# Kernel optimization log

Measured on AMD Instinct MI355X. Metric: run time of the kernel, lower is better.

## Reference

```python
import jax, jax.numpy as jnp
import numpy as np

SEQ, BATCH, NFEAT, HID = 512, 128, 64, 256


def setup_inputs() -> dict:
    key = jax.random.key(0)
    ks = jax.random.split(key, 11)
    s = 0.05
    return {
        "X": jax.random.normal(ks[0], (SEQ, BATCH, NFEAT), jnp.float32),
        "w_ih0": jax.random.normal(ks[1], (4 * HID, NFEAT), jnp.float32) * s,
        "w_hh0": jax.random.normal(ks[2], (4 * HID, HID), jnp.float32) * s,
        "b_ih0": jax.random.normal(ks[3], (4 * HID,), jnp.float32) * s,
        "b_hh0": jax.random.normal(ks[4], (4 * HID,), jnp.float32) * s,
        "w_ih1": jax.random.normal(ks[5], (4 * HID, HID), jnp.float32) * s,
        "w_hh1": jax.random.normal(ks[6], (4 * HID, HID), jnp.float32) * s,
        "b_ih1": jax.random.normal(ks[7], (4 * HID,), jnp.float32) * s,
        "b_hh1": jax.random.normal(ks[8], (4 * HID,), jnp.float32) * s,
        "fc_w": jax.random.normal(ks[9], (1, HID), jnp.float32) * s,
        "fc_b": jax.random.normal(ks[10], (1,), jnp.float32) * s,
    }


def _lstm_layer(x, w_ih, w_hh, b_ih, b_hh):
    # x: [S, B, F]; PyTorch gate order: i, f, g, o along the 4H axis.
    S, B, _ = x.shape
    H = w_hh.shape[1]
    # Precompute input projection for all timesteps (batched GEMM).
    xp = jnp.einsum("sbf,gf->sbg", x, w_ih) + b_ih + b_hh  # [S, B, 4H]
    w_hh_t = w_hh.T  # [H, 4H]

    def step(carry, xt):
        h, c = carry
        gates = xt + h @ w_hh_t  # [B, 4H]
        i, f, g, o = jnp.split(gates, 4, axis=-1)
        i = jax.nn.sigmoid(i)
        f = jax.nn.sigmoid(f)
        g = jnp.tanh(g)
        o = jax.nn.sigmoid(o)
        c = f * c + i * g
        h = o * jnp.tanh(c)
        return (h, c), h

    h0 = jnp.zeros((B, H), x.dtype)
    c0 = jnp.zeros((B, H), x.dtype)
    _, out = jax.lax.scan(step, (h0, c0), xp)
    return out  # [S, B, H]


def reference(X, w_ih0, w_hh0, b_ih0, b_hh0, w_ih1, w_hh1, b_ih1, b_hh1, fc_w, fc_b):
    out0 = _lstm_layer(X, w_ih0, w_hh0, b_ih0, b_hh0)
    out1 = _lstm_layer(out0, w_ih1, w_hh1, b_ih1, b_hh1)
    last = out1[-1]  # [B, H]
    return last @ fc_w.T + fc_b  # [B, 1]
```

## Files before the change

kernel.cpp:

```cpp
#include <hip/hip_runtime.h>

#define SEQ   512
#define BATCH 128
#define NFEAT 64
#define HID   256
#define HB    (BATCH * HID)
#define NGRP  8
#define GBLK  32


typedef __attribute__((ext_vector_type(8))) short  short8;
typedef __attribute__((ext_vector_type(4))) float  f32x4;
typedef __attribute__((ext_vector_type(4))) unsigned short us4;

__device__ __forceinline__ unsigned short f2bf(float f) {
    union { float f; unsigned u; } c; c.f = f;
    unsigned r = c.u + 0x7FFF + ((c.u >> 16) & 1);
    return (unsigned short)(r >> 16);
}
__device__ __forceinline__ float bf2f(unsigned short h) {
    union { float f; unsigned u; } c; c.u = ((unsigned)h) << 16;
    return c.f;
}

__device__ __forceinline__ float2 aload2(const float* p) {
    unsigned long long raw = __hip_atomic_load(
        (const unsigned long long*)p, __ATOMIC_RELAXED, __HIP_MEMORY_SCOPE_AGENT);
    union { unsigned long long u; float2 f; } c; c.u = raw;
    return c.f;
}
__device__ __forceinline__ void astore1(float* p, float v) {
    union { float f; unsigned u; } c; c.f = v;
    __hip_atomic_store((unsigned*)p, c.u, __ATOMIC_RELAXED, __HIP_MEMORY_SCOPE_AGENT);
}

__global__ __launch_bounds__(256, 1) void lstm_persist(
    const float* __restrict__ X,
    const float* __restrict__ w_ih0,
    const float* __restrict__ w_hh0,
    const float* __restrict__ b_ih0,
    const float* __restrict__ b_hh0,
    const float* __restrict__ w_ih1,
    const float* __restrict__ w_hh1,
    const float* __restrict__ b_ih1,
    const float* __restrict__ b_hh1,
    float* __restrict__ h0buf,
    float* __restrict__ h1buf,
    unsigned* __restrict__ flags)
{
    const int bid = blockIdx.x;
    const int tid = threadIdx.x;
    const int g     = bid >> 5;
    const int r     = bid & 31;
    const int layer = r >> 4;
    const int ct    = r & 15;
    const int b0    = g * 16;
    const int j0    = ct * 16;

    const int wave = tid >> 6;
    const int l    = tid & 63;
    const int kq   = l >> 4;
    const int ar   = l & 15;

    __shared__ __align__(16) unsigned short hsh[16 * 512];
    __shared__ __align__(16) unsigned short hsl[16 * 512];
    __shared__ float red[4][4][16][17];
    __shared__ float bbuf[4][16];

    {
        const short8 z8 = {0, 0, 0, 0, 0, 0, 0, 0};
        for (int i = tid; i < 16 * 512 / 8; i += 256) {
            ((short8*)hsh)[i] = z8;
            ((short8*)hsl)[i] = z8;
        }
    }
    if (tid < 64) {
        const int gg = tid >> 4, cc = tid & 15;
        const float* bi_ = layer ? b_ih1 : b_ih0;
        const float* bh_ = layer ? b_hh1 : b_hh0;
        bbuf[gg][cc] = bi_[gg * 256 + j0 + cc] + bh_[gg * 256 + j0 + cc];
    }

    short8 Ahi[4][4], Alo[4][4];
    {
        const short8 z8 = {0, 0, 0, 0, 0, 0, 0, 0};
        #pragma unroll
        for (int gg = 0; gg < 4; ++gg) {
            const int row = gg * 256 + j0 + ar;
            #pragma unroll
            for (int kt = 0; kt < 4; ++kt) {
                const int k = (wave * 4 + kt) * 32 + kq * 8;
                const float* src = nullptr;
                if (layer) {
                    src = (k < 256) ? (w_ih1 + (size_t)row * 256 + k)
                                    : (w_hh1 + (size_t)row * 256 + (k - 256));
                } else {
                    if (k < 64)       src = w_ih0 + (size_t)row * 64 + k;
                    else if (k < 320) src = w_hh0 + (size_t)row * 256 + (k - 64);
                }
                short8 hi8 = z8, lo8 = z8;
                if (src) {
                    const float4 a = ((const float4*)src)[0];
                    const float4 b = ((const float4*)src)[1];
                    const float wv[8] = {a.x, a.y, a.z, a.w, b.x, b.y, b.z, b.w};
                    #pragma unroll
                    for (int i = 0; i < 8; ++i) {
                        const unsigned short h = f2bf(wv[i]);
                        hi8[i] = (short)h;
                        lo8[i] = (short)f2bf(wv[i] - bf2f(h));
                    }
                }
                Ahi[gg][kt] = hi8;
                Alo[gg][kt] = lo8;
            }
        }
    }

    const int eb = tid >> 4, ecc = tid & 15;
    float creg = 0.f;

    float*    hown  = layer ? h1buf : h0buf;
    unsigned* gflag = flags + (size_t)g * GBLK * 32;

    const int pb = tid >> 4, pf = tid & 15;
    float4 xpf = make_float4(0.f, 0.f, 0.f, 0.f);
    if (!layer)
        xpf = ((const float4*)(X + (size_t)(b0 + pb) * NFEAT))[pf];

    __syncthreads();

    for (int s = 0; s <= SEQ; ++s) {
        const int  t      = layer ? (s - 1) : s;
        const bool active = layer ? (s >= 1) : (s < SEQ);

        if (active) {
            const int par = t & 1;
            const int row = tid >> 4, f0 = tid & 15;
            const int swz = (row & 7) << 3;
            {
                const int hoff = layer ? 256 : 64;
                const float* hp =
                    hown + (size_t)(par ^ 1) * HB + (size_t)(b0 + row) * HID + f0 * 16;
                float v[16];
                #pragma unroll
                for (int i = 0; i < 8; ++i) {
                    const float2 t2 = aload2(hp + 2 * i);
                    v[2 * i] = t2.x; v[2 * i + 1] = t2.y;
                }
                short8 h0v, h1v, l0v, l1v;
                #pragma unroll
                for (int i = 0; i < 8; ++i) {
                    unsigned short hh = f2bf(v[i]);
                    h0v[i] = (short)hh;
                    l0v[i] = (short)f2bf(v[i] - bf2f(hh));
                    hh = f2bf(v[i + 8]);
                    h1v[i] = (short)hh;
                    l1v[i] = (short)f2bf(v[i + 8] - bf2f(hh));
                }
                const int us = row * 512 + hoff + f0 * 16;
                *(short8*)&hsh[us ^ swz]       = h0v;
                *(short8*)&hsh[(us + 8) ^ swz] = h1v;
                *(short8*)&hsl[us ^ swz]       = l0v;
                *(short8*)&hsl[(us + 8) ^ swz] = l1v;
            }
            if (layer) {
                const float* xp =
                    h0buf + (size_t)par * HB + (size_t)(b0 + row) * HID + f0 * 16;
                float v[16];
                #pragma unroll
                for (int i = 0; i < 8; ++i) {
                    const float2 t2 = aload2(xp + 2 * i);
                    v[2 * i] = t2.x; v[2 * i + 1] = t2.y;
                }
                short8 h0v, h1v, l0v, l1v;
                #pragma unroll
                for (int i = 0; i < 8; ++i) {
                    unsigned short hh = f2bf(v[i]);
                    h0v[i] = (short)hh;
                    l0v[i] = (short)f2bf(v[i] - bf2f(hh));
                    hh = f2bf(v[i + 8]);
                    h1v[i] = (short)hh;
                    l1v[i] = (short)f2bf(v[i + 8] - bf2f(hh));
                }
                const int us = row * 512 + f0 * 16;
                *(short8*)&hsh[us ^ swz]       = h0v;
                *(short8*)&hsh[(us + 8) ^ swz] = h1v;
                *(short8*)&hsl[us ^ swz]       = l0v;
                *(short8*)&hsl[(us + 8) ^ swz] = l1v;
            } else {
                const float xv[4] = {xpf.x, xpf.y, xpf.z, xpf.w};
                us4 xh, xl;
                #pragma unroll
                for (int i = 0; i < 4; ++i) {
                    const unsigned short hh = f2bf(xv[i]);
                    xh[i] = hh;
                    xl[i] = f2bf(xv[i] - bf2f(hh));
                }
                const int us = pb * 512 + pf * 4;
                const int sw = (pb & 7) << 3;
                *(us4*)&hsh[us ^ sw] = xh;
                *(us4*)&hsl[us ^ sw] = xl;
            }
        }
        __syncthreads();

        if (!layer && t + 1 < SEQ)
            xpf = ((const float4*)(X + (size_t)(t + 1) * BATCH * NFEAT
                                     + (size_t)(b0 + pb) * NFEAT))[pf];

        if (active) {
            f32x4 acc[4];
            #pragma unroll
            for (int gg = 0; gg < 4; ++gg)
                acc[gg] = (f32x4){0.f, 0.f, 0.f, 0.f};

            #pragma unroll
            for (int kt = 0; kt < 4; ++kt) {
                const int KT = wave * 4 + kt;
                const int us = ar * 512 + KT * 32 + kq * 8;
                const int uswz = us ^ ((ar & 7) << 3);
                const short8 bh = *(const short8*)&hsh[uswz];
                const short8 bl = *(const short8*)&hsl[uswz];
                #pragma unroll
                for (int gg = 0; gg < 4; ++gg)
                    acc[gg] = __builtin_amdgcn_mfma_f32_16x16x32_bf16(
                        Ahi[gg][kt], bh, acc[gg], 0, 0, 0);
                #pragma unroll
                for (int gg = 0; gg < 4; ++gg)
                    acc[gg] = __builtin_amdgcn_mfma_f32_16x16x32_bf16(
                        Alo[gg][kt], bh, acc[gg], 0, 0, 0);
                #pragma unroll
                for (int gg = 0; gg < 4; ++gg)
                    acc[gg] = __builtin_amdgcn_mfma_f32_16x16x32_bf16(
                        Ahi[gg][kt], bl, acc[gg], 0, 0, 0);
            }
            const int crow = kq * 4;
            #pragma unroll
            for (int gg = 0; gg < 4; ++gg) {
                #pragma unroll
                for (int i = 0; i < 4; ++i)
                    red[wave][gg][crow + i][ar] = acc[gg][i];
            }
        }
        __syncthreads();

        if (active) {
            float p[4];
            #pragma unroll
            for (int gg = 0; gg < 4; ++gg)
                p[gg] = bbuf[gg][ecc] + red[0][gg][ecc][eb] + red[1][gg][ecc][eb]
                                      + red[2][gg][ecc][eb] + red[3][gg][ecc][eb];
            const float ig = 1.0f / (1.0f + __expf(-p[0]));
            const float fg = 1.0f / (1.0f + __expf(-p[1]));
            const float gg_ = tanhf(p[2]);
            const float og = 1.0f / (1.0f + __expf(-p[3]));
            creg = fg * creg + ig * gg_;
            const float hv = og * tanhf(creg);
            astore1(&hown[(size_t)(t & 1) * HB + (size_t)(b0 + eb) * HID + j0 + ecc], hv);
        }

        if (s < SEQ) {
            const unsigned rr = (unsigned)(s + 1);
            __syncthreads();
            if (tid == 0)
                __hip_atomic_store(&gflag[r * 32], rr, __ATOMIC_RELAXED,
                                   __HIP_MEMORY_SCOPE_AGENT);
            if (tid < GBLK) {
                int guard = 0;
                while (__hip_atomic_load(&gflag[tid * 32], __ATOMIC_RELAXED,
                                         __HIP_MEMORY_SCOPE_AGENT) < rr &&
                       ++guard < (1 << 26))
                    __builtin_amdgcn_s_sleep(1);
            }
            __syncthreads();
        }
    }
}

__global__ __launch_bounds__(64) void fc_kernel(
    const float* __restrict__ h1last,
    const float* __restrict__ fc_w,
    const float* __restrict__ fc_b,
    float* __restrict__ out)
{
    const int b    = blockIdx.x;
    const int lane = threadIdx.x;
    float sum = 0.0f;
    #pragma unroll
    for (int k = lane; k < HID; k += 64)
        sum += h1last[b * HID + k] * fc_w[k];
    #pragma unroll
    for (int off = 32; off > 0; off >>= 1)
        sum += __shfl_down(sum, off);
    if (lane == 0) out[b] = sum + fc_b[0];
}

extern "C" void kernel_launch(void* const* d_in, const int* in_sizes, int n_in,
                              void* d_out, int out_size, void* d_ws, size_t ws_size,
                              hipStream_t stream)
{
    const float* X     = (const float*)d_in[0];
    const float* w_ih0 = (const float*)d_in[1];
    const float* w_hh0 = (const float*)d_in[2];
    const float* b_ih0 = (const float*)d_in[3];
    const float* b_hh0 = (const float*)d_in[4];
    const float* w_ih1 = (const float*)d_in[5];
    const float* w_hh1 = (const float*)d_in[6];
    const float* b_ih1 = (const float*)d_in[7];
    const float* b_hh1 = (const float*)d_in[8];
    const float* fc_w  = (const float*)d_in[9];
    const float* fc_b  = (const float*)d_in[10];

    float*    ws    = (float*)d_ws;
    float*    h0    = ws;
    float*    h1    = ws + 2 * HB;
    unsigned* flags = (unsigned*)(ws + 4 * HB);

    const size_t zbytes = (size_t)4 * HB * sizeof(float) + NGRP * GBLK * 32 * 4;
    (void)hipMemsetAsync(d_ws, 0, zbytes, stream);

    lstm_persist<<<NGRP * GBLK, 256, 0, stream>>>(X,
        w_ih0, w_hh0, b_ih0, b_hh0,
        w_ih1, w_hh1, b_ih1, b_hh1,
        h0, h1, flags);

    fc_kernel<<<BATCH, 64, 0, stream>>>(h1 + HB, fc_w, fc_b, (float*)d_out);
}
```

Measured before the change: 2.208 ms.

## Replace group-wide flag barrier with tagged hidden-state words and dataflow waits

Removes the per-step all-block flag barrier across the 32 blocks of a batch group. Each hidden value is now stored as a 64-bit word holding the step tag and the bf16 hi/lo split. Consumers spin until every loaded word carries the expected tag, so each block waits only on the data it reads. Layer 0 waits on a small layer-1 progress counter before overwriting its double buffer, and the hi/lo conversion moves to the producer. The LDS reduction layout is also changed to allow vector writes. Risks include heavier polling traffic on the h buffers, twice the buffer size, and correctness depending on relaxed 64-bit atomic visibility and bounded spin guards.

```diff
diff --git a/kernel.cpp b/kernel.cpp
--- a/kernel.cpp
+++ b/kernel.cpp
@@ -6,9 +6,9 @@
 #define HID   256
 #define HB    (BATCH * HID)
 #define NGRP  8
-#define GBLK  32
-
-
+
+
+typedef unsigned long long u64;
 typedef __attribute__((ext_vector_type(8))) short  short8;
 typedef __attribute__((ext_vector_type(4))) float  f32x4;
 typedef __attribute__((ext_vector_type(4))) unsigned short us4;
@@ -23,15 +23,17 @@
     return c.f;
 }
 
-__device__ __forceinline__ float2 aload2(const float* p) {
-    unsigned long long raw = __hip_atomic_load(
-        (const unsigned long long*)p, __ATOMIC_RELAXED, __HIP_MEMORY_SCOPE_AGENT);
-    union { unsigned long long u; float2 f; } c; c.u = raw;
-    return c.f;
-}
-__device__ __forceinline__ void astore1(float* p, float v) {
-    union { float f; unsigned u; } c; c.f = v;
-    __hip_atomic_store((unsigned*)p, c.u, __ATOMIC_RELAXED, __HIP_MEMORY_SCOPE_AGENT);
+__device__ __forceinline__ u64 ald64(const u64* p) {
+    return __hip_atomic_load(p, __ATOMIC_RELAXED, __HIP_MEMORY_SCOPE_AGENT);
+}
+__device__ __forceinline__ void ast64(u64* p, u64 v) {
+    __hip_atomic_store(p, v, __ATOMIC_RELAXED, __HIP_MEMORY_SCOPE_AGENT);
+}
+__device__ __forceinline__ unsigned ald32(const unsigned* p) {
+    return __hip_atomic_load(p, __ATOMIC_RELAXED, __HIP_MEMORY_SCOPE_AGENT);
+}
+__device__ __forceinline__ void ast32(unsigned* p, unsigned v) {
+    __hip_atomic_store(p, v, __ATOMIC_RELAXED, __HIP_MEMORY_SCOPE_AGENT);
 }
 
 __global__ __launch_bounds__(256, 1) void lstm_persist(
@@ -44,9 +46,9 @@
     const float* __restrict__ w_hh1,
     const float* __restrict__ b_ih1,
     const float* __restrict__ b_hh1,
-    float* __restrict__ h0buf,
-    float* __restrict__ h1buf,
-    unsigned* __restrict__ flags)
+    u64* __restrict__ h0w,
+    u64* __restrict__ h1w,
+    unsigned* __restrict__ l1prog)
 {
     const int bid = blockIdx.x;
     const int tid = threadIdx.x;
@@ -64,7 +66,7 @@
 
     __shared__ __align__(16) unsigned short hsh[16 * 512];
     __shared__ __align__(16) unsigned short hsl[16 * 512];
-    __shared__ float red[4][4][16][17];
+    __shared__ float red[4][4][16][20];
     __shared__ float bbuf[4][16];
 
     {
@@ -119,8 +121,9 @@
     const int eb = tid >> 4, ecc = tid & 15;
     float creg = 0.f;
 
-    float*    hown  = layer ? h1buf : h0buf;
-    unsigned* gflag = flags + (size_t)g * GBLK * 32;
+    u64*      hown = layer ? h1w : h0w;
+    unsigned* prog = l1prog + (size_t)g * 16 * 32;
+    const int hoff = layer ? 256 : 64;
 
     const int pb = tid >> 4, pf = tid & 15;
     float4 xpf = make_float4(0.f, 0.f, 0.f, 0.f);
@@ -129,86 +132,86 @@
 
     __syncthreads();
 
-    for (int s = 0; s <= SEQ; ++s) {
-        const int  t      = layer ? (s - 1) : s;
-        const bool active = layer ? (s >= 1) : (s < SEQ);
-
-        if (active) {
-            const int par = t & 1;
-            const int row = tid >> 4, f0 = tid & 15;
-            const int swz = (row & 7) << 3;
-            {
-                const int hoff = layer ? 256 : 64;
-                const float* hp =
-                    hown + (size_t)(par ^ 1) * HB + (size_t)(b0 + row) * HID + f0 * 16;
-                float v[16];
-                #pragma unroll
-                for (int i = 0; i < 8; ++i) {
-                    const float2 t2 = aload2(hp + 2 * i);
-                    v[2 * i] = t2.x; v[2 * i + 1] = t2.y;
-                }
-                short8 h0v, h1v, l0v, l1v;
-                #pragma unroll
-                for (int i = 0; i < 8; ++i) {
-                    unsigned short hh = f2bf(v[i]);
-                    h0v[i] = (short)hh;
-                    l0v[i] = (short)f2bf(v[i] - bf2f(hh));
-                    hh = f2bf(v[i + 8]);
-                    h1v[i] = (short)hh;
-                    l1v[i] = (short)f2bf(v[i + 8] - bf2f(hh));
-                }
-                const int us = row * 512 + hoff + f0 * 16;
-                *(short8*)&hsh[us ^ swz]       = h0v;
-                *(short8*)&hsh[(us + 8) ^ swz] = h1v;
-                *(short8*)&hsl[us ^ swz]       = l0v;
-                *(short8*)&hsl[(us + 8) ^ swz] = l1v;
-            }
-            if (layer) {
-                const float* xp =
-                    h0buf + (size_t)par * HB + (size_t)(b0 + row) * HID + f0 * 16;
-                float v[16];
-                #pragma unroll
-                for (int i = 0; i < 8; ++i) {
-                    const float2 t2 = aload2(xp + 2 * i);
-                    v[2 * i] = t2.x; v[2 * i + 1] = t2.y;
-                }
-                short8 h0v, h1v, l0v, l1v;
-                #pragma unroll
-                for (int i = 0; i < 8; ++i) {
-                    unsigned short hh = f2bf(v[i]);
-                    h0v[i] = (short)hh;
-                    l0v[i] = (short)f2bf(v[i] - bf2f(hh));
-                    hh = f2bf(v[i + 8]);
-                    h1v[i] = (short)hh;
-                    l1v[i] = (short)f2bf(v[i + 8] - bf2f(hh));
-                }
-                const int us = row * 512 + f0 * 16;
-                *(short8*)&hsh[us ^ swz]       = h0v;
-                *(short8*)&hsh[(us + 8) ^ swz] = h1v;
-                *(short8*)&hsl[us ^ swz]       = l0v;
-                *(short8*)&hsl[(us + 8) ^ swz] = l1v;
-            } else {
-                const float xv[4] = {xpf.x, xpf.y, xpf.z, xpf.w};
-                us4 xh, xl;
-                #pragma unroll
-                for (int i = 0; i < 4; ++i) {
-                    const unsigned short hh = f2bf(xv[i]);
-                    xh[i] = hh;
-                    xl[i] = f2bf(xv[i] - bf2f(hh));
-                }
-                const int us = pb * 512 + pf * 4;
-                const int sw = (pb & 7) << 3;
-                *(us4*)&hsh[us ^ sw] = xh;
-                *(us4*)&hsl[us ^ sw] = xl;
-            }
+    for (int t = 0; t < SEQ; ++t) {
+        const int par = t & 1, pp = par ^ 1;
+        const int b = tid >> 4, f0 = tid & 15;
+        const int swz = (b & 7) << 3;
+
+        if (t > 0) {
+            const u64* src = hown + ((size_t)pp * BATCH + b0 + b) * HID + f0 * 16;
+            u64 v[16];
+            const unsigned wtag = (unsigned)t;
+            int guard = 0; bool ok;
+            do {
+                ok = true;
+                #pragma unroll
+                for (int i = 0; i < 16; ++i) v[i] = ald64(src + i);
+                #pragma unroll
+                for (int i = 0; i < 16; ++i) ok &= ((unsigned)(v[i] >> 32) == wtag);
+            } while (!ok && ++guard < (1 << 16));
+            short8 h0v, h1v, l0v, l1v;
+            #pragma unroll
+            for (int i = 0; i < 8; ++i) {
+                h0v[i] = (short)((v[i] >> 16) & 0xffff);
+                l0v[i] = (short)(v[i] & 0xffff);
+                h1v[i] = (short)((v[i + 8] >> 16) & 0xffff);
+                l1v[i] = (short)(v[i + 8] & 0xffff);
+            }
+            const int us = b * 512 + hoff + f0 * 16;
+            *(short8*)&hsh[us ^ swz]       = h0v;
+            *(short8*)&hsh[(us + 8) ^ swz] = h1v;
+            *(short8*)&hsl[us ^ swz]       = l0v;
+            *(short8*)&hsl[(us + 8) ^ swz] = l1v;
+        }
+        if (layer) {
+            const u64* src = h0w + ((size_t)par * BATCH + b0 + b) * HID + f0 * 16;
+            u64 v[16];
+            const unsigned wtag = (unsigned)(t + 1);
+            int guard = 0; bool ok;
+            do {
+                ok = true;
+                #pragma unroll
+                for (int i = 0; i < 16; ++i) v[i] = ald64(src + i);
+                #pragma unroll
+                for (int i = 0; i < 16; ++i) ok &= ((unsigned)(v[i] >> 32) == wtag);
+            } while (!ok && ++guard < (1 << 16));
+            short8 h0v, h1v, l0v, l1v;
+            #pragma unroll
+            for (int i = 0; i < 8; ++i) {
+                h0v[i] = (short)((v[i] >> 16) & 0xffff);
+                l0v[i] = (short)(v[i] & 0xffff);
+                h1v[i] = (short)((v[i + 8] >> 16) & 0xffff);
+                l1v[i] = (short)(v[i + 8] & 0xffff);
+            }
+            const int us = b * 512 + f0 * 16;
+            *(short8*)&hsh[us ^ swz]       = h0v;
+            *(short8*)&hsh[(us + 8) ^ swz] = h1v;
+            *(short8*)&hsl[us ^ swz]       = l0v;
+            *(short8*)&hsl[(us + 8) ^ swz] = l1v;
+        } else {
+            const float xv[4] = {xpf.x, xpf.y, xpf.z, xpf.w};
+            us4 xh, xl;
+            #pragma unroll
+            for (int i = 0; i < 4; ++i) {
+                const unsigned short hh = f2bf(xv[i]);
+                xh[i] = hh;
+                xl[i] = f2bf(xv[i] - bf2f(hh));
+            }
+            const int us = pb * 512 + pf * 4;
+            const int sw = (pb & 7) << 3;
+            *(us4*)&hsh[us ^ sw] = xh;
+            *(us4*)&hsl[us ^ sw] = xl;
         }
         __syncthreads();
 
-        if (!layer && t + 1 < SEQ)
+        if (layer) {
+            if (tid == 0) ast32(&prog[ct * 32], (unsigned)(t + 1));
+        } else if (t + 1 < SEQ) {
             xpf = ((const float4*)(X + (size_t)(t + 1) * BATCH * NFEAT
                                      + (size_t)(b0 + pb) * NFEAT))[pf];
-
-        if (active) {
+        }
+
+        {
             f32x4 acc[4];
             #pragma unroll
             for (int gg = 0; gg < 4; ++gg)
@@ -234,51 +237,46 @@
                     acc[gg] = __builtin_amdgcn_mfma_f32_16x16x32_bf16(
                         Ahi[gg][kt], bl, acc[gg], 0, 0, 0);
             }
-            const int crow = kq * 4;
-            #pragma unroll
-            for (int gg = 0; gg < 4; ++gg) {
-                #pragma unroll
-                for (int i = 0; i < 4; ++i)
-                    red[wave][gg][crow + i][ar] = acc[gg][i];
-            }
+            #pragma unroll
+            for (int gg = 0; gg < 4; ++gg)
+                *(f32x4*)&red[wave][gg][ar][kq * 4] = acc[gg];
         }
         __syncthreads();
 
-        if (active) {
+        float hv;
+        {
             float p[4];
             #pragma unroll
             for (int gg = 0; gg < 4; ++gg)
-                p[gg] = bbuf[gg][ecc] + red[0][gg][ecc][eb] + red[1][gg][ecc][eb]
-                                      + red[2][gg][ecc][eb] + red[3][gg][ecc][eb];
-            const float ig = 1.0f / (1.0f + __expf(-p[0]));
-            const float fg = 1.0f / (1.0f + __expf(-p[1]));
+                p[gg] = bbuf[gg][ecc] + red[0][gg][eb][ecc] + red[1][gg][eb][ecc]
+                                      + red[2][gg][eb][ecc] + red[3][gg][eb][ecc];
+            const float ig  = 1.0f / (1.0f + __expf(-p[0]));
+            const float fg  = 1.0f / (1.0f + __expf(-p[1]));
             const float gg_ = tanhf(p[2]);
-            const float og = 1.0f / (1.0f + __expf(-p[3]));
+            const float og  = 1.0f / (1.0f + __expf(-p[3]));
             creg = fg * creg + ig * gg_;
-            const float hv = og * tanhf(creg);
-            astore1(&hown[(size_t)(t & 1) * HB + (size_t)(b0 + eb) * HID + j0 + ecc], hv);
-        }
-
-        if (s < SEQ) {
-            const unsigned rr = (unsigned)(s + 1);
-            __syncthreads();
-            if (tid == 0)
-                __hip_atomic_store(&gflag[r * 32], rr, __ATOMIC_RELAXED,
-                                   __HIP_MEMORY_SCOPE_AGENT);
-            if (tid < GBLK) {
-                int guard = 0;
-                while (__hip_atomic_load(&gflag[tid * 32], __ATOMIC_RELAXED,
-                                         __HIP_MEMORY_SCOPE_AGENT) < rr &&
-                       ++guard < (1 << 26))
-                    __builtin_amdgcn_s_sleep(1);
-            }
-            __syncthreads();
+            hv   = og * tanhf(creg);
+        }
+
+        if (!layer && t >= 2 && tid < 16) {
+            int guard = 0;
+            while (ald32(&prog[tid * 32]) < (unsigned)(t - 1) &&
+                   ++guard < (1 << 16)) { }
+        }
+        __syncthreads();
+
+        {
+            const unsigned short hi = f2bf(hv);
+            const unsigned short lo = f2bf(hv - bf2f(hi));
+            const u64 wv = ((u64)(unsigned)(t + 1) << 32)
+                         | ((unsigned)hi << 16) | (unsigned)lo;
+            ast64(&hown[((size_t)par * BATCH + b0 + eb) * HID + j0 + ecc], wv);
         }
     }
 }
 
 __global__ __launch_bounds__(64) void fc_kernel(
-    const float* __restrict__ h1last,
+    const u64* __restrict__ h1last_w,
     const float* __restrict__ fc_w,
     const float* __restrict__ fc_b,
     float* __restrict__ out)
@@ -287,8 +285,12 @@
     const int lane = threadIdx.x;
     float sum = 0.0f;
     #pragma unroll
-    for (int k = lane; k < HID; k += 64)
-        sum += h1last[b * HID + k] * fc_w[k];
+    for (int k = lane; k < HID; k += 64) {
+        const u64 w = h1last_w[(size_t)b * HID + k];
+        const float h = bf2f((unsigned short)((w >> 16) & 0xffff))
+                      + bf2f((unsigned short)(w & 0xffff));
+        sum += h * fc_w[k];
+    }
     #pragma unroll
     for (int off = 32; off > 0; off >>= 1)
         sum += __shfl_down(sum, off);
@@ -311,18 +313,17 @@
     const float* fc_w  = (const float*)d_in[9];
     const float* fc_b  = (const float*)d_in[10];
 
-    float*    ws    = (float*)d_ws;
-    float*    h0    = ws;
-    float*    h1    = ws + 2 * HB;
-    unsigned* flags = (unsigned*)(ws + 4 * HB);
-
-    const size_t zbytes = (size_t)4 * HB * sizeof(float) + NGRP * GBLK * 32 * 4;
+    u64*      h0w    = (u64*)d_ws;
+    u64*      h1w    = h0w + 2 * HB;
+    unsigned* l1prog = (unsigned*)(h1w + 2 * HB);
+
+    const size_t zbytes = (size_t)4 * HB * sizeof(u64) + NGRP * 16 * 32 * 4;
     (void)hipMemsetAsync(d_ws, 0, zbytes, stream);
 
-    lstm_persist<<<NGRP * GBLK, 256, 0, stream>>>(X,
+    lstm_persist<<<NGRP * 32, 256, 0, stream>>>(X,
         w_ih0, w_hh0, b_ih0, b_hh0,
         w_ih1, w_hh1, b_ih1, b_hh1,
-        h0, h1, flags);
-
-    fc_kernel<<<BATCH, 64, 0, stream>>>(h1 + HB, fc_w, fc_b, (float*)d_out);
-}
+        h0w, h1w, l1prog);
+
+    fc_kernel<<<BATCH, 64, 0, stream>>>(h1w + HB, fc_w, fc_b, (float*)d_out);
+}
```

Measured after the change: 4.942 ms. 124% more time.
